# Performance work log

Hardware: AMD Instinct MI355X
Metric: run time of the kernel (lower is better)

Reference implementation:

```python
import jax, jax.numpy as jnp
import numpy as np

N_NODES = 100000
N_EDGES = 1000000
N_GRAPHS = 16
D_NODE = 64
D_EDGE = 32
D_GLOB = 32
OUT_DIM = 64
IN1 = 2 * D_NODE + D_EDGE + D_GLOB  # 192
IN2 = D_NODE + OUT_DIM + D_GLOB     # 160


def setup_inputs() -> dict:
    key = jax.random.key(0)
    ks = jax.random.split(key, 9)
    x = jax.random.normal(ks[0], (N_NODES, D_NODE), dtype=jnp.float32)
    edge_index = jax.random.randint(ks[1], (2, N_EDGES), 0, N_NODES, dtype=jnp.int64 if jax.config.jax_enable_x64 else jnp.int32)
    edge_attr = jax.random.normal(ks[2], (N_EDGES, D_EDGE), dtype=jnp.float32)
    u = jax.random.normal(ks[3], (N_GRAPHS, D_GLOB), dtype=jnp.float32)
    batch = jnp.sort(jax.random.randint(ks[4], (N_NODES,), 0, N_GRAPHS))
    # Linear params (kaiming-ish scale)
    W1 = jax.random.normal(ks[5], (IN1, OUT_DIM), dtype=jnp.float32) / np.sqrt(IN1)
    b1 = jnp.zeros((OUT_DIM,), dtype=jnp.float32)
    W2 = jax.random.normal(ks[6], (IN2, OUT_DIM), dtype=jnp.float32) / np.sqrt(IN2)
    b2 = jnp.zeros((OUT_DIM,), dtype=jnp.float32)
    return {"x": x, "edge_index": edge_index, "edge_attr": edge_attr, "u": u,
            "batch": batch, "W1": W1, "b1": b1, "W2": W2, "b2": b2}


def reference(x, edge_index, edge_attr, u, batch, W1, b1, W2, b2):
    src = edge_index[0]  # [E]
    dst = edge_index[1]  # [E]
    u_per_node = u[batch]  # [N, Du] gather globals to nodes
    # gather-concat: [E, 2D + De + Du]
    all_feat = jnp.concatenate([x[dst], x[src], edge_attr, u_per_node[dst]], axis=-1)
    # mlp_1 + ReLU on every edge message
    msg = jax.nn.relu(all_feat @ W1 + b1)  # [E, out]
    # scatter-sum to destination nodes
    agg = jax.ops.segment_sum(msg, dst, num_segments=x.shape[0])  # [N, out]
    # mlp_2 + ReLU on nodes
    node_in = jnp.concatenate([x, agg, u_per_node], axis=-1)  # [N, D + out + Du]
    return jax.nn.relu(node_in @ W2 + b2)
```

## Files before the change

### kernel.cpp

```cpp
#include <hip/hip_runtime.h>

constexpr int N_NODES = 100000;
constexpr int N_EDGES = 1000000;
constexpr int D_NODE  = 64;
constexpr int D_EDGE  = 32;
constexpr int D_GLOB  = 32;
constexpr int OUT_DIM = 64;
constexpr int K1 = 2*D_NODE + D_EDGE + D_GLOB;
constexpr int K2 = D_NODE + OUT_DIM + D_GLOB;

typedef _Float16 f16x8 __attribute__((ext_vector_type(8)));
typedef unsigned short ushort8_t __attribute__((ext_vector_type(8)));
typedef float floatx16 __attribute__((ext_vector_type(16)));

constexpr int FS = 200;

constexpr size_t WS_W1T = 0;
constexpr size_t WS_W2T = 24576;
constexpr size_t WS_UB  = 45056;
constexpr size_t WS_XB  = 46080;

__device__ inline unsigned pack_f2(float a, float b) {
    auto h = __builtin_amdgcn_cvt_pkrtz(a, b);
    return __builtin_bit_cast(unsigned, h);
}

__global__ __launch_bounds__(256) void prep_kernel(
    const float* __restrict__ x, const float* __restrict__ u,
    const float* __restrict__ W1, const float* __restrict__ W2,
    unsigned short* __restrict__ ws_w1t, unsigned short* __restrict__ ws_w2t,
    unsigned short* __restrict__ ws_ub, unsigned short* __restrict__ ws_xb)
{
    const int t = blockIdx.x * 256 + threadIdx.x;
    const int stride = gridDim.x * 256;
    const float4* x4 = (const float4*)x;
    for (int i = t; i < N_NODES * 16; i += stride) {
        float4 v = x4[i];
        uint2 pk;
        pk.x = pack_f2(v.x, v.y);
        pk.y = pack_f2(v.z, v.w);
        *(uint2*)&ws_xb[i * 4] = pk;
    }
    for (int i = t; i < K1 * 64; i += stride) {
        int k = i >> 6, n = i & 63;
        _Float16 h = (_Float16)W1[i];
        ws_w1t[n * K1 + k] = __builtin_bit_cast(unsigned short, h);
    }
    for (int i = t; i < K2 * 64; i += stride) {
        int k = i >> 6, n = i & 63;
        _Float16 h = (_Float16)W2[i];
        ws_w2t[n * K2 + k] = __builtin_bit_cast(unsigned short, h);
    }
    for (int i = t; i < 16 * D_GLOB; i += stride) {
        _Float16 h = (_Float16)u[i];
        ws_ub[i] = __builtin_bit_cast(unsigned short, h);
    }
}

__global__ __launch_bounds__(256, 6) void edge_kernel(
    const unsigned short* __restrict__ xb, const int* __restrict__ ei,
    const float* __restrict__ ea, const unsigned short* __restrict__ ub,
    const int* __restrict__ batch, const unsigned short* __restrict__ W1t,
    const float* __restrict__ b1, float* __restrict__ out)
{
    __shared__ __align__(16) unsigned short smem[64 * FS];
    __shared__ int s_dst[64];
    __shared__ int s_src[64];
    __shared__ int s_b[64];

    const int tid  = threadIdx.x;
    const int lane = tid & 63;
    const int wv   = tid >> 6;
    const int tile = blockIdx.x;
    const int eh   = wv >> 1;
    const int nh   = wv & 1;
    const int col  = lane & 31;
    const int half = lane >> 5;
    const float4* ea4 = (const float4*)ea;

    if (tid < 64) {
        int e = tile * 64 + tid;
        int d = ei[N_EDGES + e];
        s_dst[tid] = d;
        s_src[tid] = ei[e];
        s_b[tid]   = batch[d];
    }

    {
        int el = tid >> 2, c = tid & 3;
        float4 v0 = ea4[(tile*64 + el) * 8 + c * 2 + 0];
        float4 v1 = ea4[(tile*64 + el) * 8 + c * 2 + 1];
        uint4 pk;
        pk.x = pack_f2(v0.x, v0.y); pk.y = pack_f2(v0.z, v0.w);
        pk.z = pack_f2(v1.x, v1.y); pk.w = pack_f2(v1.z, v1.w);
        *(uint4*)&smem[el * FS + (16 + c) * 8] = pk;
    }

    f16x8 Wf[12];
    #pragma unroll
    for (int s = 0; s < 12; ++s)
        Wf[s] = __builtin_bit_cast(f16x8,
            *(const ushort8_t*)&W1t[(nh*32 + col) * K1 + s*16 + half*8]);

    const int chp = (lane & 31) * 2;
    const float2 bv = *(const float2*)&b1[chp];

    __syncthreads();

    for (int q = tid; q < 64 * 20; q += 256) {
        int el = q / 20;
        int c  = q - el * 20;
        uint4 pk;
        if (c < 8)       pk = *(const uint4*)&xb[s_dst[el] * 64 + c * 8];
        else if (c < 16) pk = *(const uint4*)&xb[s_src[el] * 64 + (c - 8) * 8];
        else             pk = *(const uint4*)&ub[s_b[el] * 32 + (c - 16) * 8];
        *(uint4*)&smem[el * FS + (c < 16 ? c : c + 4) * 8] = pk;
    }
    __syncthreads();

    floatx16 acc = {0,0,0,0,0,0,0,0,0,0,0,0,0,0,0,0};
    #pragma unroll
    for (int s = 0; s < 12; ++s) {
        f16x8 a = __builtin_bit_cast(f16x8,
            *(const ushort8_t*)&smem[(eh*32 + col) * FS + s*16 + half*8]);
        acc = __builtin_amdgcn_mfma_f32_32x32x16_f16(a, Wf[s], acc, 0, 0, 0);
    }

    __syncthreads();
    float* smemf = (float*)smem;
    #pragma unroll
    for (int r = 0; r < 16; ++r) {
        int e = eh*32 + (r & 3) + 8*(r >> 2) + 4*half;
        smemf[e * 64 + nh*32 + col] = acc[r];
    }
    __syncthreads();

    #pragma unroll
    for (int it = 0; it < 8; ++it) {
        int e = wv*16 + it*2 + half;
        float2 m = *(const float2*)&smemf[e * 64 + chp];
        float v0 = m.x + bv.x; v0 = v0 > 0.f ? v0 : 0.f;
        float v1 = m.y + bv.y; v1 = v1 > 0.f ? v1 : 0.f;
        unsigned pk = pack_f2(v0, v1);
        unsigned short* p = (unsigned short*)out + (size_t)s_dst[e] * 128 + chp;
        asm volatile("global_atomic_pk_add_f16 %0, %1, off"
                     :: "v"(p), "v"(pk) : "memory");
    }
}

__global__ __launch_bounds__(256, 6) void node_kernel(
    const unsigned short* __restrict__ xb, const unsigned short* __restrict__ ub,
    const int* __restrict__ batch, const unsigned short* __restrict__ W2t,
    const float* __restrict__ b2, float* __restrict__ out)
{
    __shared__ __align__(16) unsigned short smem[64 * FS];
    __shared__ int s_b[64];

    const int tid  = threadIdx.x;
    const int lane = tid & 63;
    const int wv   = tid >> 6;
    const int base = blockIdx.x * 64;
    const int eh   = wv >> 1;
    const int nh   = wv & 1;
    const int col  = lane & 31;
    const int half = lane >> 5;

    if (tid < 64) {
        int n = base + tid;
        s_b[tid] = (n < N_NODES) ? batch[n] : 0;
    }

    f16x8 Bf[10];
    #pragma unroll
    for (int s = 0; s < 10; ++s)
        Bf[s] = __builtin_bit_cast(f16x8,
            *(const ushort8_t*)&W2t[(nh*32 + col) * K2 + s*16 + half*8]);
    const float b2v = b2[nh*32 + col];

    __syncthreads();

    const unsigned short* aggb = (const unsigned short*)out;
    for (int q = tid; q < 64 * 20; q += 256) {
        int nl = q / 20;
        int c  = q - nl * 20;
        int n  = base + nl;
        uint4 pk;
        if (n >= N_NODES) pk = uint4{0, 0, 0, 0};
        else if (c < 8)   pk = *(const uint4*)&xb[n * 64 + c * 8];
        else if (c < 16)  pk = *(const uint4*)&aggb[(size_t)n * 128 + (c - 8) * 8];
        else              pk = *(const uint4*)&ub[s_b[nl] * 32 + (c - 16) * 8];
        *(uint4*)&smem[nl * FS + c * 8] = pk;
    }
    __syncthreads();

    floatx16 acc = {0,0,0,0,0,0,0,0,0,0,0,0,0,0,0,0};
    #pragma unroll
    for (int s = 0; s < 10; ++s) {
        f16x8 a = __builtin_bit_cast(f16x8,
            *(const ushort8_t*)&smem[(eh*32 + col) * FS + s*16 + half*8]);
        acc = __builtin_amdgcn_mfma_f32_32x32x16_f16(a, Bf[s], acc, 0, 0, 0);
    }

    #pragma unroll
    for (int r = 0; r < 16; ++r) {
        int n = base + eh*32 + (r & 3) + 8*(r >> 2) + 4*half;
        if (n < N_NODES) {
            float vv = acc[r] + b2v;
            out[n * 64 + nh*32 + col] = vv > 0.f ? vv : 0.f;
        }
    }
}

extern "C" void kernel_launch(void* const* d_in, const int* in_sizes, int n_in,
                              void* d_out, int out_size, void* d_ws, size_t ws_size,
                              hipStream_t stream) {
    const float* x     = (const float*)d_in[0];
    const int*   ei    = (const int*)d_in[1];
    const float* ea    = (const float*)d_in[2];
    const float* u     = (const float*)d_in[3];
    const int*   batch = (const int*)d_in[4];
    const float* W1    = (const float*)d_in[5];
    const float* b1    = (const float*)d_in[6];
    const float* W2    = (const float*)d_in[7];
    const float* b2    = (const float*)d_in[8];
    float* out = (float*)d_out;

    unsigned short* ws_w1t = (unsigned short*)((char*)d_ws + WS_W1T);
    unsigned short* ws_w2t = (unsigned short*)((char*)d_ws + WS_W2T);
    unsigned short* ws_ub  = (unsigned short*)((char*)d_ws + WS_UB);
    unsigned short* ws_xb  = (unsigned short*)((char*)d_ws + WS_XB);

    (void)hipMemsetAsync(out, 0, (size_t)out_size * sizeof(float), stream);

    prep_kernel<<<2048, 256, 0, stream>>>(x, u, W1, W2, ws_w1t, ws_w2t, ws_ub, ws_xb);
    edge_kernel<<<N_EDGES / 64, 256, 0, stream>>>(ws_xb, ei, ea, ws_ub, batch, ws_w1t, b1, out);
    node_kernel<<<(N_NODES + 63) / 64, 256, 0, stream>>>(ws_xb, ws_ub, batch, ws_w2t, b2, out);
}
```

Baseline: 363.2 us.

## Fuse prep, edge and node kernels into one persistent cooperative kernel

Merges the memset, prep, edge and node kernels into a single persistent kernel launched cooperatively. Grid-wide syncs separate the phases, and blocks loop over edge and node tiles. This removes three kernel launches plus the memset and loads the weight fragments once per block instead of once per tile. In exchange it adds grid-sync costs and caps parallelism at the resident block count, which may reduce latency hiding on the gather-heavy edge phase. A three-launch fallback handles the case where the cooperative launch fails.

```diff
diff --git a/kernel.cpp b/kernel.cpp
--- a/kernel.cpp
+++ b/kernel.cpp
@@ -1,4 +1,7 @@
 #include <hip/hip_runtime.h>
+#include <hip/hip_cooperative_groups.h>
+
+namespace cg = cooperative_groups;
 
 constexpr int N_NODES = 100000;
 constexpr int N_EDGES = 1000000;
@@ -25,43 +28,15 @@
     return __builtin_bit_cast(unsigned, h);
 }
 
-__global__ __launch_bounds__(256) void prep_kernel(
-    const float* __restrict__ x, const float* __restrict__ u,
-    const float* __restrict__ W1, const float* __restrict__ W2,
-    unsigned short* __restrict__ ws_w1t, unsigned short* __restrict__ ws_w2t,
-    unsigned short* __restrict__ ws_ub, unsigned short* __restrict__ ws_xb)
-{
-    const int t = blockIdx.x * 256 + threadIdx.x;
-    const int stride = gridDim.x * 256;
-    const float4* x4 = (const float4*)x;
-    for (int i = t; i < N_NODES * 16; i += stride) {
-        float4 v = x4[i];
-        uint2 pk;
-        pk.x = pack_f2(v.x, v.y);
-        pk.y = pack_f2(v.z, v.w);
-        *(uint2*)&ws_xb[i * 4] = pk;
-    }
-    for (int i = t; i < K1 * 64; i += stride) {
-        int k = i >> 6, n = i & 63;
-        _Float16 h = (_Float16)W1[i];
-        ws_w1t[n * K1 + k] = __builtin_bit_cast(unsigned short, h);
-    }
-    for (int i = t; i < K2 * 64; i += stride) {
-        int k = i >> 6, n = i & 63;
-        _Float16 h = (_Float16)W2[i];
-        ws_w2t[n * K2 + k] = __builtin_bit_cast(unsigned short, h);
-    }
-    for (int i = t; i < 16 * D_GLOB; i += stride) {
-        _Float16 h = (_Float16)u[i];
-        ws_ub[i] = __builtin_bit_cast(unsigned short, h);
-    }
-}
-
-__global__ __launch_bounds__(256, 6) void edge_kernel(
-    const unsigned short* __restrict__ xb, const int* __restrict__ ei,
-    const float* __restrict__ ea, const unsigned short* __restrict__ ub,
-    const int* __restrict__ batch, const unsigned short* __restrict__ W1t,
-    const float* __restrict__ b1, float* __restrict__ out)
+__global__ __launch_bounds__(256, 6) void fused_all(
+    const float* __restrict__ x, const int* __restrict__ ei,
+    const float* __restrict__ ea, const float* __restrict__ u,
+    const int* __restrict__ batch,
+    const float* __restrict__ W1, const float* __restrict__ b1,
+    const float* __restrict__ W2, const float* __restrict__ b2,
+    unsigned short* __restrict__ w1t, unsigned short* __restrict__ w2t,
+    unsigned short* __restrict__ ub, unsigned short* __restrict__ xb,
+    float* __restrict__ out, int phase)
 {
     __shared__ __align__(16) unsigned short smem[64 * FS];
     __shared__ int s_dst[64];
@@ -71,142 +46,166 @@
     const int tid  = threadIdx.x;
     const int lane = tid & 63;
     const int wv   = tid >> 6;
-    const int tile = blockIdx.x;
     const int eh   = wv >> 1;
     const int nh   = wv & 1;
     const int col  = lane & 31;
     const int half = lane >> 5;
-    const float4* ea4 = (const float4*)ea;
-
-    if (tid < 64) {
-        int e = tile * 64 + tid;
-        int d = ei[N_EDGES + e];
-        s_dst[tid] = d;
-        s_src[tid] = ei[e];
-        s_b[tid]   = batch[d];
-    }
-
-    {
-        int el = tid >> 2, c = tid & 3;
-        float4 v0 = ea4[(tile*64 + el) * 8 + c * 2 + 0];
-        float4 v1 = ea4[(tile*64 + el) * 8 + c * 2 + 1];
-        uint4 pk;
-        pk.x = pack_f2(v0.x, v0.y); pk.y = pack_f2(v0.z, v0.w);
-        pk.z = pack_f2(v1.x, v1.y); pk.w = pack_f2(v1.z, v1.w);
-        *(uint4*)&smem[el * FS + (16 + c) * 8] = pk;
-    }
-
-    f16x8 Wf[12];
-    #pragma unroll
-    for (int s = 0; s < 12; ++s)
-        Wf[s] = __builtin_bit_cast(f16x8,
-            *(const ushort8_t*)&W1t[(nh*32 + col) * K1 + s*16 + half*8]);
-
-    const int chp = (lane & 31) * 2;
-    const float2 bv = *(const float2*)&b1[chp];
-
-    __syncthreads();
-
-    for (int q = tid; q < 64 * 20; q += 256) {
-        int el = q / 20;
-        int c  = q - el * 20;
-        uint4 pk;
-        if (c < 8)       pk = *(const uint4*)&xb[s_dst[el] * 64 + c * 8];
-        else if (c < 16) pk = *(const uint4*)&xb[s_src[el] * 64 + (c - 8) * 8];
-        else             pk = *(const uint4*)&ub[s_b[el] * 32 + (c - 16) * 8];
-        *(uint4*)&smem[el * FS + (c < 16 ? c : c + 4) * 8] = pk;
-    }
-    __syncthreads();
-
-    floatx16 acc = {0,0,0,0,0,0,0,0,0,0,0,0,0,0,0,0};
-    #pragma unroll
-    for (int s = 0; s < 12; ++s) {
-        f16x8 a = __builtin_bit_cast(f16x8,
-            *(const ushort8_t*)&smem[(eh*32 + col) * FS + s*16 + half*8]);
-        acc = __builtin_amdgcn_mfma_f32_32x32x16_f16(a, Wf[s], acc, 0, 0, 0);
-    }
-
-    __syncthreads();
-    float* smemf = (float*)smem;
-    #pragma unroll
-    for (int r = 0; r < 16; ++r) {
-        int e = eh*32 + (r & 3) + 8*(r >> 2) + 4*half;
-        smemf[e * 64 + nh*32 + col] = acc[r];
-    }
-    __syncthreads();
-
-    #pragma unroll
-    for (int it = 0; it < 8; ++it) {
-        int e = wv*16 + it*2 + half;
-        float2 m = *(const float2*)&smemf[e * 64 + chp];
-        float v0 = m.x + bv.x; v0 = v0 > 0.f ? v0 : 0.f;
-        float v1 = m.y + bv.y; v1 = v1 > 0.f ? v1 : 0.f;
-        unsigned pk = pack_f2(v0, v1);
-        unsigned short* p = (unsigned short*)out + (size_t)s_dst[e] * 128 + chp;
-        asm volatile("global_atomic_pk_add_f16 %0, %1, off"
-                     :: "v"(p), "v"(pk) : "memory");
-    }
-}
-
-__global__ __launch_bounds__(256, 6) void node_kernel(
-    const unsigned short* __restrict__ xb, const unsigned short* __restrict__ ub,
-    const int* __restrict__ batch, const unsigned short* __restrict__ W2t,
-    const float* __restrict__ b2, float* __restrict__ out)
-{
-    __shared__ __align__(16) unsigned short smem[64 * FS];
-    __shared__ int s_b[64];
-
-    const int tid  = threadIdx.x;
-    const int lane = tid & 63;
-    const int wv   = tid >> 6;
-    const int base = blockIdx.x * 64;
-    const int eh   = wv >> 1;
-    const int nh   = wv & 1;
-    const int col  = lane & 31;
-    const int half = lane >> 5;
-
-    if (tid < 64) {
-        int n = base + tid;
-        s_b[tid] = (n < N_NODES) ? batch[n] : 0;
-    }
-
-    f16x8 Bf[10];
-    #pragma unroll
-    for (int s = 0; s < 10; ++s)
-        Bf[s] = __builtin_bit_cast(f16x8,
-            *(const ushort8_t*)&W2t[(nh*32 + col) * K2 + s*16 + half*8]);
-    const float b2v = b2[nh*32 + col];
-
-    __syncthreads();
-
-    const unsigned short* aggb = (const unsigned short*)out;
-    for (int q = tid; q < 64 * 20; q += 256) {
-        int nl = q / 20;
-        int c  = q - nl * 20;
-        int n  = base + nl;
-        uint4 pk;
-        if (n >= N_NODES) pk = uint4{0, 0, 0, 0};
-        else if (c < 8)   pk = *(const uint4*)&xb[n * 64 + c * 8];
-        else if (c < 16)  pk = *(const uint4*)&aggb[(size_t)n * 128 + (c - 8) * 8];
-        else              pk = *(const uint4*)&ub[s_b[nl] * 32 + (c - 16) * 8];
-        *(uint4*)&smem[nl * FS + c * 8] = pk;
-    }
-    __syncthreads();
-
-    floatx16 acc = {0,0,0,0,0,0,0,0,0,0,0,0,0,0,0,0};
-    #pragma unroll
-    for (int s = 0; s < 10; ++s) {
-        f16x8 a = __builtin_bit_cast(f16x8,
-            *(const ushort8_t*)&smem[(eh*32 + col) * FS + s*16 + half*8]);
-        acc = __builtin_amdgcn_mfma_f32_32x32x16_f16(a, Bf[s], acc, 0, 0, 0);
-    }
-
-    #pragma unroll
-    for (int r = 0; r < 16; ++r) {
-        int n = base + eh*32 + (r & 3) + 8*(r >> 2) + 4*half;
-        if (n < N_NODES) {
-            float vv = acc[r] + b2v;
-            out[n * 64 + nh*32 + col] = vv > 0.f ? vv : 0.f;
+    const int gsz  = gridDim.x * 256;
+    const int gt   = blockIdx.x * 256 + tid;
+
+    if (phase <= 0) {
+        const float4* x4 = (const float4*)x;
+        for (int i = gt; i < N_NODES * 16; i += gsz) {
+            float4 v = x4[i];
+            uint2 pk;
+            pk.x = pack_f2(v.x, v.y);
+            pk.y = pack_f2(v.z, v.w);
+            *(uint2*)&xb[i * 4] = pk;
+        }
+        const uint4 z = {0, 0, 0, 0};
+        uint4* o4 = (uint4*)out;
+        for (int i = gt; i < N_NODES * 16; i += gsz)
+            o4[i] = z;
+        for (int i = gt; i < K1 * 64; i += gsz) {
+            int k = i >> 6, n = i & 63;
+            _Float16 h = (_Float16)W1[i];
+            w1t[n * K1 + k] = __builtin_bit_cast(unsigned short, h);
+        }
+        for (int i = gt; i < K2 * 64; i += gsz) {
+            int k = i >> 6, n = i & 63;
+            _Float16 h = (_Float16)W2[i];
+            w2t[n * K2 + k] = __builtin_bit_cast(unsigned short, h);
+        }
+        for (int i = gt; i < 16 * D_GLOB; i += gsz) {
+            _Float16 h = (_Float16)u[i];
+            ub[i] = __builtin_bit_cast(unsigned short, h);
+        }
+    }
+    if (phase == -1) { __threadfence(); cg::this_grid().sync(); }
+
+    if (phase == -1 || phase == 1) {
+        const float4* ea4 = (const float4*)ea;
+
+        f16x8 Wf[12];
+        #pragma unroll
+        for (int s = 0; s < 12; ++s)
+            Wf[s] = __builtin_bit_cast(f16x8,
+                *(const ushort8_t*)&w1t[(nh*32 + col) * K1 + s*16 + half*8]);
+        const int chp = (lane & 31) * 2;
+        const float2 bv = *(const float2*)&b1[chp];
+
+        for (int tile = blockIdx.x; tile < N_EDGES / 64; tile += gridDim.x) {
+            __syncthreads();
+
+            if (tid < 64) {
+                int e = tile * 64 + tid;
+                int d = ei[N_EDGES + e];
+                s_dst[tid] = d;
+                s_src[tid] = ei[e];
+                s_b[tid]   = batch[d];
+            }
+            {
+                int el = tid >> 2, c = tid & 3;
+                float4 v0 = ea4[(tile*64 + el) * 8 + c * 2 + 0];
+                float4 v1 = ea4[(tile*64 + el) * 8 + c * 2 + 1];
+                uint4 pk;
+                pk.x = pack_f2(v0.x, v0.y); pk.y = pack_f2(v0.z, v0.w);
+                pk.z = pack_f2(v1.x, v1.y); pk.w = pack_f2(v1.z, v1.w);
+                *(uint4*)&smem[el * FS + (16 + c) * 8] = pk;
+            }
+            __syncthreads();
+
+            for (int q = tid; q < 64 * 20; q += 256) {
+                int el = q / 20;
+                int c  = q - el * 20;
+                uint4 pk;
+                if (c < 8)       pk = *(const uint4*)&xb[s_dst[el] * 64 + c * 8];
+                else if (c < 16) pk = *(const uint4*)&xb[s_src[el] * 64 + (c - 8) * 8];
+                else             pk = *(const uint4*)&ub[s_b[el] * 32 + (c - 16) * 8];
+                *(uint4*)&smem[el * FS + (c < 16 ? c : c + 4) * 8] = pk;
+            }
+            __syncthreads();
+
+            floatx16 acc = {0,0,0,0,0,0,0,0,0,0,0,0,0,0,0,0};
+            #pragma unroll
+            for (int s = 0; s < 12; ++s) {
+                f16x8 a = __builtin_bit_cast(f16x8,
+                    *(const ushort8_t*)&smem[(eh*32 + col) * FS + s*16 + half*8]);
+                acc = __builtin_amdgcn_mfma_f32_32x32x16_f16(a, Wf[s], acc, 0, 0, 0);
+            }
+
+            __syncthreads();
+            float* smemf = (float*)smem;
+            #pragma unroll
+            for (int r = 0; r < 16; ++r) {
+                int e = eh*32 + (r & 3) + 8*(r >> 2) + 4*half;
+                smemf[e * 64 + nh*32 + col] = acc[r];
+            }
+            __syncthreads();
+
+            #pragma unroll
+            for (int it = 0; it < 8; ++it) {
+                int e = wv*16 + it*2 + half;
+                float2 m = *(const float2*)&smemf[e * 64 + chp];
+                float v0 = m.x + bv.x; v0 = v0 > 0.f ? v0 : 0.f;
+                float v1 = m.y + bv.y; v1 = v1 > 0.f ? v1 : 0.f;
+                unsigned pk = pack_f2(v0, v1);
+                unsigned short* p = (unsigned short*)out + (size_t)s_dst[e] * 128 + chp;
+                asm volatile("global_atomic_pk_add_f16 %0, %1, off"
+                             :: "v"(p), "v"(pk) : "memory");
+            }
+        }
+    }
+    if (phase == -1) { __threadfence(); cg::this_grid().sync(); }
+
+    if (phase == -1 || phase == 2) {
+        f16x8 Bf[10];
+        #pragma unroll
+        for (int s = 0; s < 10; ++s)
+            Bf[s] = __builtin_bit_cast(f16x8,
+                *(const ushort8_t*)&w2t[(nh*32 + col) * K2 + s*16 + half*8]);
+        const float b2v = b2[nh*32 + col];
+        const unsigned short* aggb = (const unsigned short*)out;
+
+        for (int t = blockIdx.x; t < (N_NODES + 63) / 64; t += gridDim.x) {
+            const int base = t * 64;
+            __syncthreads();
+
+            if (tid < 64) {
+                int n = base + tid;
+                s_b[tid] = (n < N_NODES) ? batch[n] : 0;
+            }
+            __syncthreads();
+
+            for (int q = tid; q < 64 * 20; q += 256) {
+                int nl = q / 20;
+                int c  = q - nl * 20;
+                int n  = base + nl;
+                uint4 pk;
+                if (n >= N_NODES) pk = uint4{0, 0, 0, 0};
+                else if (c < 8)   pk = *(const uint4*)&xb[n * 64 + c * 8];
+                else if (c < 16)  pk = *(const uint4*)&aggb[(size_t)n * 128 + (c - 8) * 8];
+                else              pk = *(const uint4*)&ub[s_b[nl] * 32 + (c - 16) * 8];
+                *(uint4*)&smem[nl * FS + c * 8] = pk;
+            }
+            __syncthreads();
+
+            floatx16 acc = {0,0,0,0,0,0,0,0,0,0,0,0,0,0,0,0};
+            #pragma unroll
+            for (int s = 0; s < 10; ++s) {
+                f16x8 a = __builtin_bit_cast(f16x8,
+                    *(const ushort8_t*)&smem[(eh*32 + col) * FS + s*16 + half*8]);
+                acc = __builtin_amdgcn_mfma_f32_32x32x16_f16(a, Bf[s], acc, 0, 0, 0);
+            }
+
+            #pragma unroll
+            for (int r = 0; r < 16; ++r) {
+                int n = base + eh*32 + (r & 3) + 8*(r >> 2) + 4*half;
+                if (n < N_NODES) {
+                    float vv = acc[r] + b2v;
+                    out[(size_t)n * 64 + nh*32 + col] = vv > 0.f ? vv : 0.f;
+                }
+            }
         }
     }
 }
@@ -230,9 +229,34 @@
     unsigned short* ws_ub  = (unsigned short*)((char*)d_ws + WS_UB);
     unsigned short* ws_xb  = (unsigned short*)((char*)d_ws + WS_XB);
 
-    (void)hipMemsetAsync(out, 0, (size_t)out_size * sizeof(float), stream);
-
-    prep_kernel<<<2048, 256, 0, stream>>>(x, u, W1, W2, ws_w1t, ws_w2t, ws_ub, ws_xb);
-    edge_kernel<<<N_EDGES / 64, 256, 0, stream>>>(ws_xb, ei, ea, ws_ub, batch, ws_w1t, b1, out);
-    node_kernel<<<(N_NODES + 63) / 64, 256, 0, stream>>>(ws_xb, ws_ub, batch, ws_w2t, b2, out);
+    static int g_blocks = 0;
+    if (g_blocks == 0) {
+        int maxb = 0;
+        if (hipOccupancyMaxActiveBlocksPerMultiprocessor(&maxb, fused_all, 256, 0)
+                != hipSuccess || maxb <= 0)
+            maxb = 4;
+        if (maxb > 6) maxb = 6;
+        int cus = 256;
+        hipDeviceProp_t prop;
+        if (hipGetDeviceProperties(&prop, 0) == hipSuccess && prop.multiProcessorCount > 0)
+            cus = prop.multiProcessorCount;
+        g_blocks = cus * maxb;
+    }
+
+    int phase = -1;
+    void* args[] = { (void*)&x, (void*)&ei, (void*)&ea, (void*)&u, (void*)&batch,
+                     (void*)&W1, (void*)&b1, (void*)&W2, (void*)&b2,
+                     (void*)&ws_w1t, (void*)&ws_w2t, (void*)&ws_ub, (void*)&ws_xb,
+                     (void*)&out, (void*)&phase };
+    hipError_t err = hipLaunchCooperativeKernel(fused_all, dim3(g_blocks), dim3(256),
+                                                args, 0, stream);
+    if (err != hipSuccess) {
+        (void)hipGetLastError();
+        fused_all<<<g_blocks, 256, 0, stream>>>(x, ei, ea, u, batch, W1, b1, W2, b2,
+                                                ws_w1t, ws_w2t, ws_ub, ws_xb, out, 0);
+        fused_all<<<g_blocks, 256, 0, stream>>>(x, ei, ea, u, batch, W1, b1, W2, b2,
+                                                ws_w1t, ws_w2t, ws_ub, ws_xb, out, 1);
+        fused_all<<<g_blocks, 256, 0, stream>>>(x, ei, ea, u, batch, W1, b1, W2, b2,
+                                                ws_w1t, ws_w2t, ws_ub, ws_xb, out, 2);
+    }
 }
```

Measured after the change: 740.1 us. +103.8%, slower.
